# Optimization experiments

Measured on AMD Instinct MI355X. Metric: run time of the kernel, lower is better.

The kernel has to match this reference:

```python
import jax, jax.numpy as jnp
from jax import lax
import numpy as np

STEP = 5          # 10 / hz with hz = 2
H = 256           # n_hidden_after_deconv
B = 128
T = 4096


def _segment_indices(lengths):
    """Static (host-side) ragged segment bookkeeping.
    For each sample: hz2_index = sorted {L - 5j >= 0} -> segments [r+5k : r+5(k+1)],
    r = L % 5, k = 0..L//5-1. Returns flat batch idx, [N,5] time idx, per-sample
    segment position idx, and seg counts."""
    lengths = np.asarray(lengths)
    segs = (lengths // STEP).astype(np.int64)
    b_idx = np.repeat(np.arange(lengths.shape[0]), segs)
    starts = np.concatenate([
        (int(L) % STEP) + STEP * np.arange(int(s)) for L, s in zip(lengths, segs)
    ])
    s_idx = np.concatenate([np.arange(int(s)) for s in segs])
    t_idx = starts[:, None] + np.arange(STEP)[None, :]
    return b_idx, t_idx, s_idx, segs


def setup_inputs() -> dict:
    key = jax.random.key(0)
    ks = jax.random.split(key, 10)
    trajectory = jax.random.normal(ks[0], (B, T, 3), jnp.float32) * 10.0
    traj_length = jax.random.randint(ks[1], (B,), 2048, T + 1)
    sc = 0.05
    return {
        'trajectory': trajectory,
        'traj_length': traj_length,
        'conv1_w': jax.random.normal(ks[2], (H, 3, 3), jnp.float32) * sc,
        'conv1_b': jnp.zeros((H,), jnp.float32),
        'conv2_w': jax.random.normal(ks[3], (H, H, 3), jnp.float32) * sc,
        'conv2_b': jnp.zeros((H,), jnp.float32),
        'w_ih': jax.random.normal(ks[4], (3 * H, H), jnp.float32) * sc,
        'w_hh': jax.random.normal(ks[5], (3 * H, H), jnp.float32) * sc,
        'b_ih': jnp.zeros((3 * H,), jnp.float32),
        'b_hh': jnp.zeros((3 * H,), jnp.float32),
    }


def _forward(trajectory, traj_length, conv1_w, conv1_b, conv2_w, conv2_b,
             w_ih, w_hh, b_ih, b_hh):
    lengths = np.asarray(traj_length)
    b_idx, t_idx, s_idx, segs = _segment_indices(lengths)
    smax = int(segs.max())
    nb = trajectory.shape[0]

    # --- per-sample rotate/translate to last-frame egocentric coords ---
    end = jnp.asarray(lengths - 1)
    last = trajectory[jnp.arange(nb), end]            # [B,3]
    origin = last[:, :2]
    heading = -last[:, 2]                              # degrees
    th = jnp.deg2rad(heading)
    c, s = jnp.cos(th)[:, None], jnp.sin(th)[:, None]
    xy = trajectory[:, :, :2] - origin[:, None, :]
    xr = c * xy[..., 0] - s * xy[..., 1]
    yr = s * xy[..., 0] + c * xy[..., 1]
    ang = jnp.deg2rad(jnp.fmod(trajectory[:, :, 2] + heading[:, None] + 720.0, 360.0))
    ang = jnp.where(ang > jnp.pi, ang - 2.0 * jnp.pi, ang)
    traj_rot = jnp.stack([xr, yr, ang], axis=-1)       # [B,T,3]

    # --- batched ragged segment gather: [N,STEP,3] ---
    enc_in = traj_rot[b_idx[:, None], t_idx]
    x = jnp.transpose(enc_in, (0, 2, 1))               # [N,3,STEP]

    # --- Encoder: conv1d stack + mean pool -> [N,H] ---
    dn = ('NCW', 'OIW', 'NCW')
    x = jax.nn.relu(lax.conv_general_dilated(x, conv1_w, (1,), 'SAME',
                                             dimension_numbers=dn)
                    + conv1_b[None, :, None])
    x = jax.nn.relu(lax.conv_general_dilated(x, conv2_w, (1,), 'SAME',
                                             dimension_numbers=dn)
                    + conv2_b[None, :, None])
    ar_in = jnp.mean(x, axis=-1)                       # [N,H]

    # --- pack ragged segments to [B,Smax,H] ---
    rep_in = jnp.zeros((nb, smax, H), ar_in.dtype).at[b_idx, s_idx].set(ar_in)
    mask = jnp.zeros((nb, smax), bool).at[b_idx, s_idx].set(True)

    def gru_step(h, inp):
        x_t, m_t = inp
        gx = x_t @ w_ih.T + b_ih
        gh = h @ w_hh.T + b_hh
        xr_, xz_, xn_ = jnp.split(gx, 3, axis=-1)
        hr_, hz_, hn_ = jnp.split(gh, 3, axis=-1)
        r = jax.nn.sigmoid(xr_ + hr_)
        z = jax.nn.sigmoid(xz_ + hz_)
        n = jnp.tanh(xn_ + r * hn_)
        h_new = (1.0 - z) * n + z * h
        h_new = jnp.where(m_t[:, None], h_new, h)
        return h_new, h_new

    h0 = jnp.zeros((nb, H), ar_in.dtype)
    _, outs = lax.scan(gru_step, h0,
                       (jnp.swapaxes(rep_in, 0, 1), jnp.swapaxes(mask, 0, 1)))
    representation = jnp.swapaxes(outs, 0, 1)          # [B,Smax,H]

    # --- repres_batch: cat of representation[i, :seg_length[i]] ---
    return representation[b_idx, s_idx]                # [N,H]


def reference(trajectory, traj_length, conv1_w, conv1_b, conv2_w, conv2_b,
              w_ih, w_hh, b_ih, b_hh):
    return _forward(trajectory, traj_length, conv1_w, conv1_b, conv2_w,
                    conv2_b, w_ih, w_hh, b_ih, b_hh)
```

## Files before the change

### kernel.cpp

```cpp
#include <hip/hip_runtime.h>
#include <hip/hip_bf16.h>
#include <hip/hip_fp16.h>

#define NB 128
#define TT 4096
#define HH 256
#define G3 768
#define STEPW 5
#define PI_F 3.14159265358979323846f
#define D2R  0.017453292519943295f

typedef _Float16 f16x8 __attribute__((ext_vector_type(8)));
typedef _Float16 f16x2 __attribute__((ext_vector_type(2)));
typedef float f32x4 __attribute__((ext_vector_type(4)));

__device__ __forceinline__ unsigned int pack_f16(float x, float y){
  union { f16x2 h; unsigned int u; } cv;
  cv.h = (f16x2){(_Float16)x, (_Float16)y};
  return cv.u;
}

__device__ __forceinline__ float dot2h(unsigned int a, unsigned int b, float c){
  union { unsigned int u; f16x2 h; } ua, ub;
  ua.u = a; ub.u = b;
  return __builtin_amdgcn_fdot2(ua.h, ub.h, c, false);
}

__global__ void k_setup(const float* __restrict__ traj, const int* __restrict__ lens,
                        int* offs, int* rmod, float* cB, float* sB,
                        float* oxB, float* oyB, float* hdB){
  __shared__ int sl[NB];
  int b = threadIdx.x;
  if (b < NB) {
    int L = lens[b];
    rmod[b] = L % STEPW;
    sl[b] = L / STEPW;
    const float* last = traj + ((size_t)b*TT + (size_t)(L-1))*3;
    float ox = last[0], oy = last[1], hd = -last[2];
    float th = hd * D2R;
    cB[b] = cosf(th); sB[b] = sinf(th);
    oxB[b]=ox; oyB[b]=oy; hdB[b]=hd;
  }
  __syncthreads();
  if (threadIdx.x == 0) {
    int acc = 0;
    for (int i=0;i<NB;i++){ offs[i]=acc; acc += sl[i]; }
    offs[NB]=acc;
  }
}

__global__ void k_prep(const float* __restrict__ w2, const float* __restrict__ wih,
                       const float* __restrict__ w1,
                       _Float16* w2h, _Float16* wihh, _Float16* w1h){
  int i = blockIdx.x*256 + threadIdx.x;
  int o = i / 768; int rem = i - o*768;
  int tap = rem >> 8; int ch = rem & 255;
  w2h[i]  = (_Float16)w2[o*768 + ch*3 + tap];
  wihh[i] = (_Float16)wih[i];
  if (i < 256*32) {
    int oo = i >> 5, k = i & 31;
    float v = 0.f;
    if (k < 9) { int tp = k/3, ic = k - 3*tp; v = w1[oo*9 + ic*3 + tp]; }
    w1h[i] = (_Float16)v;
  }
}

__launch_bounds__(256, 2)
__global__ void k_conv(const float* __restrict__ traj, const int* __restrict__ offs,
                       const int* __restrict__ rmod,
                       const float* __restrict__ cB, const float* __restrict__ sB,
                       const float* __restrict__ oxB, const float* __restrict__ oyB,
                       const float* __restrict__ hdB,
                       const float* __restrict__ b1, const float* __restrict__ b2,
                       const float* __restrict__ bih, const float* __restrict__ bhh,
                       const _Float16* __restrict__ w1h,
                       const _Float16* __restrict__ w2h,
                       const _Float16* __restrict__ wihh,
                       _Float16* __restrict__ gx, int N)
{
  __shared__ __align__(16) union {
    _Float16 y1p[16][7][264];
    _Float16 sY2[80][264];
  } U;
  __shared__ __align__(16) union {
    _Float16 sA[80][32];
    _Float16 arb[16][264];
  } V;
  __shared__ float xls[16][5][3];
  __shared__ int   segB[16], segT0[16];
  __shared__ float segC[16], segS[16], segOx[16], segOy[16], segHd[16];

  const int tid = threadIdx.x;
  const int n0  = blockIdx.x * 16;
  const int cnt = min(16, N - n0);

  for (int i = tid; i < 1056; i += 256) {
    int s = i / 66, r = i - s*66;
    int wq = (r < 33) ? 0 : 6, c8 = (r < 33) ? r : r - 33;
    *(uint4*)&U.y1p[s][wq][c8*8] = make_uint4(0,0,0,0);
  }

  if (tid < 16) {
    int n = n0 + min(tid, cnt-1);
    int lo=0, hi=NB-1;
    while (lo < hi) { int mid=(lo+hi+1)>>1; if (offs[mid] <= n) lo=mid; else hi=mid-1; }
    int b = lo; int k = n - offs[b];
    segB[tid]=b; segT0[tid]= rmod[b] + STEPW*k;
    segC[tid]=cB[b]; segS[tid]=sB[b]; segOx[tid]=oxB[b]; segOy[tid]=oyB[b]; segHd[tid]=hdB[b];
  }
  __syncthreads();

  if (tid < 80) {
    int s = tid/5, w = tid%5;
    int b = segB[s]; int t = segT0[s] + w;
    const float* p = traj + ((size_t)b*TT + (size_t)t)*3;
    float X=p[0], Y=p[1], A=p[2];
    float dx = X - segOx[s], dy = Y - segOy[s];
    float c = segC[s], sn = segS[s];
    float ang = fmodf(A + segHd[s] + 720.0f, 360.0f) * D2R;
    if (ang > PI_F) ang -= 2.0f*PI_F;
    xls[s][w][0] = c*dx - sn*dy;
    xls[s][w][1] = sn*dx + c*dy;
    xls[s][w][2] = ang;
  }
  __syncthreads();

  for (int u = 0; u < 10; u++) {
    int e = u*256 + tid;
    int row = e >> 5, k = e & 31;
    float v = 0.f;
    if (k < 9) {
      int tp = k/3, ic = k - 3*tp;
      int s = row/5, w = row - 5*s;
      int wp = w + tp - 1;
      if (wp >= 0 && wp < 5) v = xls[s][wp][ic];
    }
    V.sA[0][e] = (_Float16)v;
  }
  __syncthreads();

  const int wv_  = tid >> 6;
  const int lane = tid & 63;
  const int m = lane & 15, q = lane >> 4;

  {
    f32x4 c1[5][4];
    #pragma unroll
    for (int a=0;a<5;a++) for (int bq=0;bq<4;bq++) c1[a][bq] = (f32x4){0.f,0.f,0.f,0.f};
    f16x8 bfr[4];
    #pragma unroll
    for (int nn=0;nn<4;nn++) {
      int col = (wv_*4+nn)*16 + m;
      bfr[nn] = *(const f16x8*)(w1h + col*32 + q*8);
    }
    #pragma unroll
    for (int mt=0; mt<5; mt++) {
      f16x8 afr = *(const f16x8*)&V.sA[mt*16 + m][q*8];
      #pragma unroll
      for (int nn=0;nn<4;nn++)
        c1[mt][nn] = __builtin_amdgcn_mfma_f32_16x16x32_f16(afr, bfr[nn], c1[mt][nn], 0,0,0);
    }
    #pragma unroll
    for (int nn=0;nn<4;nn++){
      int col = (wv_*4+nn)*16 + m;
      float bb = b1[col];
      #pragma unroll
      for (int mt=0;mt<5;mt++){
        #pragma unroll
        for (int v=0;v<4;v++){
          int row = mt*16 + q*4 + v;
          int s = row/5, w = row - 5*s;
          U.y1p[s][w+1][col] = (_Float16)fmaxf(c1[mt][nn][v] + bb, 0.f);
        }
      }
    }
  }
  __syncthreads();

  f32x4 acc[5][4];
  #pragma unroll
  for (int a=0;a<5;a++) for (int bq=0;bq<4;bq++) acc[a][bq] = (f32x4){0.f,0.f,0.f,0.f};
  int segi[5], wwi[5];
  #pragma unroll
  for (int mt=0; mt<5; mt++){ int row = mt*16+m; segi[mt]=row/5; wwi[mt]=row%5; }

  for (int ks=0; ks<24; ks++) {
    int tap = ks >> 3, ch0 = (ks & 7)*32 + q*8;
    f16x8 afr[5];
    #pragma unroll
    for (int mt=0; mt<5; mt++)
      afr[mt] = *(const f16x8*)&U.y1p[segi[mt]][wwi[mt]+tap][ch0];
    #pragma unroll
    for (int nn=0; nn<4; nn++) {
      int col = (wv_*4+nn)*16 + m;
      f16x8 bfr = *(const f16x8*)(w2h + (size_t)col*768 + tap*256 + (ks&7)*32 + q*8);
      #pragma unroll
      for (int mt=0; mt<5; mt++)
        acc[mt][nn] = __builtin_amdgcn_mfma_f32_16x16x32_f16(afr[mt], bfr, acc[mt][nn], 0,0,0);
    }
  }
  __syncthreads();

  #pragma unroll
  for (int nn=0;nn<4;nn++){
    int col = (wv_*4+nn)*16 + m;
    float bb = b2[col];
    #pragma unroll
    for (int mt=0;mt<5;mt++){
      #pragma unroll
      for (int v=0;v<4;v++){
        int row = mt*16 + q*4 + v;
        U.sY2[row][col] = (_Float16)fmaxf(acc[mt][nn][v] + bb, 0.f);
      }
    }
  }
  __syncthreads();

  for (int s=0; s<16; s++) {
    float sum = 0.f;
    #pragma unroll
    for (int w=0;w<5;w++) sum += (float)U.sY2[5*s+w][tid];
    V.arb[s][tid] = (_Float16)(sum*0.2f);
  }
  __syncthreads();

  f32x4 acc2[12];
  #pragma unroll
  for (int a=0;a<12;a++) acc2[a] = (f32x4){0.f,0.f,0.f,0.f};
  #pragma unroll
  for (int ks=0; ks<8; ks++) {
    int ch0 = ks*32 + q*8;
    f16x8 afr = *(const f16x8*)&V.arb[m][ch0];
    #pragma unroll
    for (int nn=0; nn<12; nn++) {
      int col = (wv_*12+nn)*16 + m;
      f16x8 bfr = *(const f16x8*)(wihh + (size_t)col*256 + ch0);
      acc2[nn] = __builtin_amdgcn_mfma_f32_16x16x32_f16(afr, bfr, acc2[nn], 0,0,0);
    }
  }
  #pragma unroll
  for (int nn=0; nn<12; nn++){
    int col = (wv_*12+nn)*16 + m;
    float bias = bih[col] + (col < 512 ? bhh[col] : 0.f);
    #pragma unroll
    for (int v=0; v<4; v++){
      int row = q*4 + v;
      if (row < cnt)
        gx[(size_t)(n0+row)*G3 + col] = (_Float16)(acc2[nn][v] + bias);
    }
  }
}

__launch_bounds__(768, 3)
__global__ void k_gru(const _Float16* __restrict__ gx,
                      const float* __restrict__ whh,
                      const float* __restrict__ bhh,
                      const int* __restrict__ offs, float* __restrict__ out)
{
  __shared__ float sPart[4][G3];
  __shared__ __align__(16) unsigned int hb[HH/2];

  const int tid  = threadIdx.x;
  const int lane = tid & 63;
  const int wv   = tid >> 6;
  const int kq   = wv & 3;
  const int rg   = wv >> 2;
  const int b    = blockIdx.x;
  const int base = offs[b];
  const int segs = offs[b+1] - base;

  unsigned int wpk[4][32];
  #pragma unroll
  for (int i=0;i<4;i++){
    const float4* wr = (const float4*)(whh + (size_t)(rg*256 + 64*i + lane)*256 + kq*64);
    #pragma unroll
    for (int c=0;c<16;c++){
      float4 v = wr[c];
      wpk[i][2*c]   = pack_f16(v.x, v.y);
      wpk[i][2*c+1] = pack_f16(v.z, v.w);
    }
  }

  const bool gate = (tid < HH);
  const float bhh2 = gate ? bhh[512+tid] : 0.f;
  float hprev = 0.f;

  if (tid < HH/2) hb[tid] = 0u;
  __syncthreads();

  float gr=0.f, gz=0.f, gn=0.f;
  if (gate) {
    const _Float16* g0 = gx + (size_t)base*G3;
    gr = (float)g0[tid]; gz = (float)g0[256+tid]; gn = (float)g0[512+tid];
  }

  for (int j=0; j<segs; j++) {
    float pr=0.f, pz=0.f, pn=0.f;
    if (gate) {
      int jn = (j+1 < segs) ? j+1 : j;
      const _Float16* g1 = gx + (size_t)(base+jn)*G3;
      pr = (float)g1[tid]; pz = (float)g1[256+tid]; pn = (float)g1[512+tid];
    }

    float a0=0.f, a1=0.f, a2=0.f, a3=0.f;
    const uint4* h4 = (const uint4*)(hb + kq*32);
    #pragma unroll
    for (int c8=0;c8<8;c8++){
      uint4 hv = h4[c8];
      #pragma unroll
      for (int t2=0;t2<4;t2++){
        unsigned int hvv = (&hv.x)[t2];
        int c = 4*c8 + t2;
        a0 = dot2h(hvv, wpk[0][c], a0);
        a1 = dot2h(hvv, wpk[1][c], a1);
        a2 = dot2h(hvv, wpk[2][c], a2);
        a3 = dot2h(hvv, wpk[3][c], a3);
      }
    }
    sPart[kq][rg*256 +        lane] = a0;
    sPart[kq][rg*256 +  64 +  lane] = a1;
    sPart[kq][rg*256 + 128 +  lane] = a2;
    sPart[kq][rg*256 + 192 +  lane] = a3;
    __syncthreads();

    if (gate) {
      float hr = sPart[0][tid]     + sPart[1][tid]     + sPart[2][tid]     + sPart[3][tid];
      float hz = sPart[0][256+tid] + sPart[1][256+tid] + sPart[2][256+tid] + sPart[3][256+tid];
      float hn = sPart[0][512+tid] + sPart[1][512+tid] + sPart[2][512+tid] + sPart[3][512+tid];
      float r = 1.f/(1.f + __expf(-(gr + hr)));
      float z = 1.f/(1.f + __expf(-(gz + hz)));
      float pre = gn + r*(hn + bhh2);
      float e2 = __expf(2.f*pre);
      float n = 1.f - 2.f/(e2 + 1.f);
      float hnew = (1.f - z)*n + z*hprev;
      hprev = hnew;
      ((_Float16*)hb)[tid] = (_Float16)hnew;
      out[(size_t)(base + j)*HH + tid] = hnew;
    }
    __syncthreads();
    gr = pr; gz = pz; gn = pn;
  }
}

extern "C" void kernel_launch(void* const* d_in, const int* in_sizes, int n_in,
                              void* d_out, int out_size, void* d_ws, size_t ws_size,
                              hipStream_t stream)
{
  const float* traj = (const float*)d_in[0];
  const int*   lens = (const int*)d_in[1];
  const float* w1   = (const float*)d_in[2];
  const float* b1   = (const float*)d_in[3];
  const float* w2   = (const float*)d_in[4];
  const float* b2   = (const float*)d_in[5];
  const float* wih  = (const float*)d_in[6];
  const float* whh  = (const float*)d_in[7];
  const float* bih  = (const float*)d_in[8];
  const float* bhh  = (const float*)d_in[9];
  float* out = (float*)d_out;
  const int N = out_size / HH;

  char* ws = (char*)d_ws;
  int*   offs = (int*)(ws + 0);
  int*   rmod = (int*)(ws + 1024);
  float* cB   = (float*)(ws + 2048);
  float* sB   = (float*)(ws + 2560);
  float* oxB  = (float*)(ws + 3072);
  float* oyB  = (float*)(ws + 3584);
  float* hdB  = (float*)(ws + 4096);
  _Float16* w1h  = (_Float16*)(ws + 8192);
  _Float16* w2h  = (_Float16*)(ws + 24576);
  _Float16* wihh = (_Float16*)(ws + 24576 + 393216);
  _Float16* gx   = (_Float16*)(ws + 24576 + 2*393216);

  k_setup<<<1, 128, 0, stream>>>(traj, lens, offs, rmod, cB, sB, oxB, oyB, hdB);
  k_prep<<<768, 256, 0, stream>>>(w2, wih, w1, w2h, wihh, w1h);
  k_conv<<<(N+15)/16, 256, 0, stream>>>(traj, offs, rmod, cB, sB, oxB, oyB, hdB,
                                        b1, b2, bih, bhh, w1h, w2h, wihh, gx, N);
  k_gru<<<NB, 768, 0, stream>>>(gx, whh, bhh, offs, out);
}
```

Before: 1.605 ms.

## Prepack GRU recurrent weights in prep kernel and prefetch MFMA B fragments

The prep kernel now converts w_hh to packed fp16 pairs in a per-thread layout, so each k_gru thread loads its weight slice with 32 contiguous uint4 loads instead of converting fp32 at startup. In k_conv, the B-operand fragments for both the conv2 and the input-projection MFMA loops are software-pipelined: the next k-step's weights are loaded while the current MFMAs run. The launch bounds attribute is replaced with explicit amdgpu waves-per-EU settings. This adds register pressure for the prefetch buffers and a larger workspace.

```diff
diff --git a/kernel.cpp b/kernel.cpp
--- a/kernel.cpp
+++ b/kernel.cpp
@@ -50,8 +50,9 @@
 }
 
 __global__ void k_prep(const float* __restrict__ w2, const float* __restrict__ wih,
-                       const float* __restrict__ w1,
-                       _Float16* w2h, _Float16* wihh, _Float16* w1h){
+                       const float* __restrict__ w1, const float* __restrict__ whh,
+                       _Float16* w2h, _Float16* wihh, _Float16* w1h,
+                       unsigned int* whhp){
   int i = blockIdx.x*256 + threadIdx.x;
   int o = i / 768; int rem = i - o*768;
   int tap = rem >> 8; int ch = rem & 255;
@@ -62,6 +63,15 @@
     float v = 0.f;
     if (k < 9) { int tp = k/3, ic = k - 3*tp; v = w1[oo*9 + ic*3 + tp]; }
     w1h[i] = (_Float16)v;
+  }
+  if (i < 98304) {
+    int tid = i >> 7, r7 = i & 127;
+    int ii = r7 >> 5, c = r7 & 31;
+    int lane = tid & 63, wvv = tid >> 6;
+    int kq = wvv & 3, rg = wvv >> 2;
+    int row = rg*256 + 64*ii + lane;
+    int kk = kq*64 + 2*c;
+    whhp[i] = pack_f16(whh[row*256 + kk], whh[row*256 + kk + 1]);
   }
 }
 
@@ -184,20 +194,33 @@
   #pragma unroll
   for (int mt=0; mt<5; mt++){ int row = mt*16+m; segi[mt]=row/5; wwi[mt]=row%5; }
 
+  f16x8 bcur[4];
+  #pragma unroll
+  for (int nn=0;nn<4;nn++) {
+    int col = (wv_*4+nn)*16 + m;
+    bcur[nn] = *(const f16x8*)(w2h + (size_t)col*768 + q*8);
+  }
   for (int ks=0; ks<24; ks++) {
     int tap = ks >> 3, ch0 = (ks & 7)*32 + q*8;
+    f16x8 bnext[4];
+    int ksn = (ks+1 < 24) ? ks+1 : ks;
+    int kofN = (ksn >> 3)*256 + (ksn & 7)*32 + q*8;
+    #pragma unroll
+    for (int nn=0;nn<4;nn++) {
+      int col = (wv_*4+nn)*16 + m;
+      bnext[nn] = *(const f16x8*)(w2h + (size_t)col*768 + kofN);
+    }
     f16x8 afr[5];
     #pragma unroll
     for (int mt=0; mt<5; mt++)
       afr[mt] = *(const f16x8*)&U.y1p[segi[mt]][wwi[mt]+tap][ch0];
     #pragma unroll
-    for (int nn=0; nn<4; nn++) {
-      int col = (wv_*4+nn)*16 + m;
-      f16x8 bfr = *(const f16x8*)(w2h + (size_t)col*768 + tap*256 + (ks&7)*32 + q*8);
+    for (int nn=0; nn<4; nn++)
       #pragma unroll
       for (int mt=0; mt<5; mt++)
-        acc[mt][nn] = __builtin_amdgcn_mfma_f32_16x16x32_f16(afr[mt], bfr, acc[mt][nn], 0,0,0);
-    }
+        acc[mt][nn] = __builtin_amdgcn_mfma_f32_16x16x32_f16(afr[mt], bcur[nn], acc[mt][nn], 0,0,0);
+    #pragma unroll
+    for (int nn=0;nn<4;nn++) bcur[nn] = bnext[nn];
   }
   __syncthreads();
 
@@ -227,16 +250,28 @@
   f32x4 acc2[12];
   #pragma unroll
   for (int a=0;a<12;a++) acc2[a] = (f32x4){0.f,0.f,0.f,0.f};
+  f16x8 bcur2[12];
+  #pragma unroll
+  for (int nn=0;nn<12;nn++) {
+    int col = (wv_*12+nn)*16 + m;
+    bcur2[nn] = *(const f16x8*)(wihh + (size_t)col*256 + q*8);
+  }
   #pragma unroll
   for (int ks=0; ks<8; ks++) {
     int ch0 = ks*32 + q*8;
+    f16x8 bnext2[12];
+    int ksn = (ks+1 < 8) ? ks+1 : ks;
+    #pragma unroll
+    for (int nn=0;nn<12;nn++) {
+      int col = (wv_*12+nn)*16 + m;
+      bnext2[nn] = *(const f16x8*)(wihh + (size_t)col*256 + ksn*32 + q*8);
+    }
     f16x8 afr = *(const f16x8*)&V.arb[m][ch0];
     #pragma unroll
-    for (int nn=0; nn<12; nn++) {
-      int col = (wv_*12+nn)*16 + m;
-      f16x8 bfr = *(const f16x8*)(wihh + (size_t)col*256 + ch0);
-      acc2[nn] = __builtin_amdgcn_mfma_f32_16x16x32_f16(afr, bfr, acc2[nn], 0,0,0);
-    }
+    for (int nn=0; nn<12; nn++)
+      acc2[nn] = __builtin_amdgcn_mfma_f32_16x16x32_f16(afr, bcur2[nn], acc2[nn], 0,0,0);
+    #pragma unroll
+    for (int nn=0;nn<12;nn++) bcur2[nn] = bnext2[nn];
   }
   #pragma unroll
   for (int nn=0; nn<12; nn++){
@@ -251,11 +286,11 @@
   }
 }
 
-__launch_bounds__(768, 3)
-__global__ void k_gru(const _Float16* __restrict__ gx,
-                      const float* __restrict__ whh,
-                      const float* __restrict__ bhh,
-                      const int* __restrict__ offs, float* __restrict__ out)
+__global__ void __attribute__((amdgpu_flat_work_group_size(768, 768), amdgpu_waves_per_eu(3, 3)))
+k_gru(const _Float16* __restrict__ gx,
+      const unsigned int* __restrict__ whhp,
+      const float* __restrict__ bhh,
+      const int* __restrict__ offs, float* __restrict__ out)
 {
   __shared__ float sPart[4][G3];
   __shared__ __align__(16) unsigned int hb[HH/2];
@@ -269,16 +304,11 @@
   const int base = offs[b];
   const int segs = offs[b+1] - base;
 
-  unsigned int wpk[4][32];
-  #pragma unroll
-  for (int i=0;i<4;i++){
-    const float4* wr = (const float4*)(whh + (size_t)(rg*256 + 64*i + lane)*256 + kq*64);
-    #pragma unroll
-    for (int c=0;c<16;c++){
-      float4 v = wr[c];
-      wpk[i][2*c]   = pack_f16(v.x, v.y);
-      wpk[i][2*c+1] = pack_f16(v.z, v.w);
-    }
+  uint4 wq4[32];
+  {
+    const uint4* wp = (const uint4*)whhp + (size_t)tid*32;
+    #pragma unroll
+    for (int c4=0;c4<32;c4++) wq4[c4] = wp[c4];
   }
 
   const bool gate = (tid < HH);
@@ -307,14 +337,14 @@
     #pragma unroll
     for (int c8=0;c8<8;c8++){
       uint4 hv = h4[c8];
+      uint4 w0 = wq4[c8], w1 = wq4[8+c8], w2 = wq4[16+c8], w3 = wq4[24+c8];
       #pragma unroll
       for (int t2=0;t2<4;t2++){
         unsigned int hvv = (&hv.x)[t2];
-        int c = 4*c8 + t2;
-        a0 = dot2h(hvv, wpk[0][c], a0);
-        a1 = dot2h(hvv, wpk[1][c], a1);
-        a2 = dot2h(hvv, wpk[2][c], a2);
-        a3 = dot2h(hvv, wpk[3][c], a3);
+        a0 = dot2h(hvv, (&w0.x)[t2], a0);
+        a1 = dot2h(hvv, (&w1.x)[t2], a1);
+        a2 = dot2h(hvv, (&w2.x)[t2], a2);
+        a3 = dot2h(hvv, (&w3.x)[t2], a3);
       }
     }
     sPart[kq][rg*256 +        lane] = a0;
@@ -367,14 +397,15 @@
   float* oxB  = (float*)(ws + 3072);
   float* oyB  = (float*)(ws + 3584);
   float* hdB  = (float*)(ws + 4096);
-  _Float16* w1h  = (_Float16*)(ws + 8192);
-  _Float16* w2h  = (_Float16*)(ws + 24576);
-  _Float16* wihh = (_Float16*)(ws + 24576 + 393216);
-  _Float16* gx   = (_Float16*)(ws + 24576 + 2*393216);
+  _Float16*     w1h  = (_Float16*)(ws + 8192);
+  _Float16*     w2h  = (_Float16*)(ws + 24576);
+  _Float16*     wihh = (_Float16*)(ws + 24576 + 393216);
+  unsigned int* whhp = (unsigned int*)(ws + 24576 + 2*393216);
+  _Float16*     gx   = (_Float16*)(ws + 24576 + 3*393216);
 
   k_setup<<<1, 128, 0, stream>>>(traj, lens, offs, rmod, cB, sB, oxB, oyB, hdB);
-  k_prep<<<768, 256, 0, stream>>>(w2, wih, w1, w2h, wihh, w1h);
+  k_prep<<<768, 256, 0, stream>>>(w2, wih, w1, whh, w2h, wihh, w1h, whhp);
   k_conv<<<(N+15)/16, 256, 0, stream>>>(traj, offs, rmod, cB, sB, oxB, oyB, hdB,
                                         b1, b2, bih, bhh, w1h, w2h, wihh, gx, N);
-  k_gru<<<NB, 768, 0, stream>>>(gx, whh, bhh, offs, out);
-}
+  k_gru<<<NB, 768, 0, stream>>>(gx, whhp, bhh, offs, out);
+}
```

Result: faster. 1.482 ms (-7.7%).
